# Kernel tuning notes

Hardware: AMD Instinct MI355X
Metric: run time of the kernel (lower is better)

The kernel has to match this reference:

```python
import jax, jax.numpy as jnp
import numpy as np

B, SEQ, PRED, T = 16, 768, 256, 1024
ENC_IN, MARK, D, H, DH = 7, 4, 512, 8, 64
BUCKET, NH, NB = 32, 4, 32          # NB = T // BUCKET (must be even)
DFF, NLAYERS, COUT = 2048, 2, 7
DEC_LEN = 512
MASK_SELF = -5e4                    # reformer TOKEN_SELF_ATTN_VALUE


def setup_inputs():
    key = jax.random.key(0)
    ks = jax.random.split(key, 16)
    s = 0.02
    return {
        "x_enc": jax.random.normal(ks[0], (B, SEQ, ENC_IN), jnp.float32),
        "x_mark_enc": jax.random.normal(ks[1], (B, SEQ, MARK), jnp.float32),
        "x_dec": jax.random.normal(ks[2], (B, DEC_LEN, ENC_IN), jnp.float32),
        "x_mark_dec": jax.random.normal(ks[3], (B, DEC_LEN, MARK), jnp.float32),
        "conv_w": jax.random.normal(ks[4], (D, ENC_IN, 3), jnp.float32) * s,
        "mark_w": jax.random.normal(ks[5], (MARK, D), jnp.float32) * s,
        "qk_w": jax.random.normal(ks[6], (NLAYERS, D, D), jnp.float32) * s,
        "v_w": jax.random.normal(ks[7], (NLAYERS, D, D), jnp.float32) * s,
        "out_w": jax.random.normal(ks[8], (NLAYERS, D, D), jnp.float32) * s,
        "out_b": jnp.zeros((NLAYERS, D), jnp.float32),
        "ln1_g": jnp.ones((NLAYERS, D), jnp.float32),
        "ln1_b": jnp.zeros((NLAYERS, D), jnp.float32),
        "ln2_g": jnp.ones((NLAYERS, D), jnp.float32),
        "ln2_b": jnp.zeros((NLAYERS, D), jnp.float32),
        "ffn_w1": jax.random.normal(ks[9], (NLAYERS, D, DFF), jnp.float32) * s,
        "ffn_b1": jnp.zeros((NLAYERS, DFF), jnp.float32),
        "ffn_w2": jax.random.normal(ks[10], (NLAYERS, DFF, D), jnp.float32) * s,
        "ffn_b2": jnp.zeros((NLAYERS, D), jnp.float32),
        "lnf_g": jnp.ones((D,), jnp.float32),
        "lnf_b": jnp.zeros((D,), jnp.float32),
        "proj_w": jax.random.normal(ks[11], (D, COUT), jnp.float32) * s,
        "proj_b": jnp.zeros((COUT,), jnp.float32),
        "rotations": jax.random.normal(ks[12], (NLAYERS, DH, NH, NB // 2), jnp.float32),
    }


def _layernorm(x, g, b):
    m = x.mean(-1, keepdims=True)
    v = ((x - m) ** 2).mean(-1, keepdims=True)
    return (x - m) / jnp.sqrt(v + 1e-5) * g + b


def _look_one_back(x):
    # concat each chunk with the previous chunk along the within-chunk axis
    return jnp.concatenate([x, jnp.roll(x, 1, axis=1)], axis=2)


def _lsh_attention(qk, v, rot):
    # shared-QK Reformer LSH attention. qk, v: [bh, t, dh]; rot: [dh, NH, NB//2]
    bh, t, d = qk.shape
    nb = t // BUCKET
    rv = jnp.einsum('btf,fhi->bhti', qk, rot)
    rv = jnp.concatenate([rv, -rv], axis=-1)
    buckets = jnp.argmax(rv, axis=-1) + (jnp.arange(NH) * nb)[None, :, None]
    buckets = buckets.reshape(bh, NH * t)                        # [bh, NH*t]
    ticker = jnp.arange(NH * t) % t
    sticker = jnp.argsort(buckets * t + ticker[None, :], axis=-1)
    undo = jnp.argsort(sticker, axis=-1)
    st = sticker % t                                             # source token ids
    sqk = jnp.take_along_axis(qk, st[..., None], axis=1)         # [bh, NH*t, d]
    sv = jnp.take_along_axis(v, st[..., None], axis=1)
    nc = NH * nb                                                 # number of chunks
    bq = sqk.reshape(bh, nc, BUCKET, d)
    bk = bq / jnp.maximum(jnp.linalg.norm(bq, axis=-1, keepdims=True), 1e-12)
    bv = sv.reshape(bh, nc, BUCKET, d)
    bk, bv = _look_one_back(bk), _look_one_back(bv)
    bq_t = st.reshape(bh, nc, BUCKET)
    bkv_t = _look_one_back(bq_t)
    dots = jnp.einsum('bcie,bcje->bcij', bq, bk) * (d ** -0.5)
    dots = jnp.where(bq_t[..., :, None] == bkv_t[..., None, :], MASK_SELF, dots)
    lse = jax.nn.logsumexp(dots, axis=-1, keepdims=True)
    bo = jnp.einsum('bcij,bcje->bcie', jnp.exp(dots - lse), bv)
    so = bo.reshape(bh, NH * t, d)
    sl = lse.reshape(bh, NH * t)
    o = jnp.take_along_axis(so, undo[..., None], axis=1).reshape(bh, NH, t, d)
    logits = jnp.take_along_axis(sl, undo, axis=1).reshape(bh, NH, t, 1)
    return (o * jax.nn.softmax(logits, axis=1)).sum(axis=1)      # [bh, t, d]


def _lsh_self_attn(x, wqk, wv, wo, bo, rot):
    b, t, _ = x.shape
    qk = (x @ wqk).reshape(b, t, H, DH).transpose(0, 2, 1, 3).reshape(b * H, t, DH)
    v = (x @ wv).reshape(b, t, H, DH).transpose(0, 2, 1, 3).reshape(b * H, t, DH)
    o = _lsh_attention(qk, v, rot)
    o = o.reshape(b, H, t, DH).transpose(0, 2, 1, 3).reshape(b, t, D)
    return o @ wo + bo


def _pos_emb(t, d):
    pos = jnp.arange(t, dtype=jnp.float32)[:, None]
    div = jnp.exp(jnp.arange(0, d, 2, dtype=jnp.float32) * (-np.log(10000.0) / d))
    pe = jnp.zeros((t, d), jnp.float32)
    return pe.at[:, 0::2].set(jnp.sin(pos * div)).at[:, 1::2].set(jnp.cos(pos * div))


def _token_emb(x, w):
    # circular Conv1d(enc_in -> d_model, kernel=3, pad=1, no bias)
    t = x.shape[1]
    xp = jnp.concatenate([x[:, -1:], x, x[:, :1]], axis=1)
    return sum(jnp.einsum('bti,oi->bto', xp[:, k:k + t], w[:, :, k]) for k in range(3))


def _forward(x_enc, x_mark_enc, x_dec, x_mark_dec, conv_w, mark_w, qk_w, v_w,
             out_w, out_b, ln1_g, ln1_b, ln2_g, ln2_b, ffn_w1, ffn_b1,
             ffn_w2, ffn_b2, lnf_g, lnf_b, proj_w, proj_b, rotations):
    x = jnp.concatenate([x_enc, x_dec[:, -PRED:, :]], axis=1)       # [B, T, enc_in]
    xm = jnp.concatenate([x_mark_enc, x_mark_dec[:, -PRED:, :]], axis=1)
    h = _token_emb(x, conv_w) + xm @ mark_w + _pos_emb(T, D)[None]  # [B, T, D]
    for l in range(NLAYERS):
        a = _lsh_self_attn(h, qk_w[l], v_w[l], out_w[l], out_b[l], rotations[l])
        h = _layernorm(h + a, ln1_g[l], ln1_b[l])
        y = jax.nn.gelu(h @ ffn_w1[l] + ffn_b1[l], approximate=False) @ ffn_w2[l] + ffn_b2[l]
        h = _layernorm(h + y, ln2_g[l], ln2_b[l])
    h = _layernorm(h, lnf_g, lnf_b)
    out = h @ proj_w + proj_b
    return out[:, -PRED:, :]


def reference(x_enc, x_mark_enc, x_dec, x_mark_dec, conv_w, mark_w, qk_w, v_w,
              out_w, out_b, ln1_g, ln1_b, ln2_g, ln2_b, ffn_w1, ffn_b1,
              ffn_w2, ffn_b2, lnf_g, lnf_b, proj_w, proj_b, rotations):
    return _forward(x_enc, x_mark_enc, x_dec, x_mark_dec, conv_w, mark_w, qk_w, v_w,
                    out_w, out_b, ln1_g, ln1_b, ln2_g, ln2_b, ffn_w1, ffn_b1,
                    ffn_w2, ffn_b2, lnf_g, lnf_b, proj_w, proj_b, rotations)
```

## Files before the change

kernel.cpp:

```cpp
#include <hip/hip_runtime.h>
#include <math.h>

#define T_ 1024
#define NT_ 4096
#define MASKSELF64 -50000.0
#define MASKSELF32 -50000.0f

__global__ __launch_bounds__(256)
void embed_kernel(const float* __restrict__ x_enc, const float* __restrict__ x_mark_enc,
                  const float* __restrict__ x_dec, const float* __restrict__ x_mark_dec,
                  const float* __restrict__ conv_w, const float* __restrict__ mark_w,
                  double* __restrict__ h) {
  int bt = blockIdx.x;
  int b = bt >> 10, t = bt & 1023;
  __shared__ double xs[3][7];
  __shared__ double xm[4];
  int tid = threadIdx.x;
  if (tid < 21) {
    int k = tid / 7, i = tid % 7;
    int tt = t + k - 1;
    if (tt < 0) tt += 1024;
    if (tt >= 1024) tt -= 1024;
    xs[k][i] = (double)((tt < 768) ? x_enc[((size_t)b*768 + tt)*7 + i]
                                   : x_dec[((size_t)b*512 + (tt - 512))*7 + i]);
  }
  if (tid >= 32 && tid < 36) {
    int m = tid - 32;
    xm[m] = (double)((t < 768) ? x_mark_enc[((size_t)b*768 + t)*4 + m]
                               : x_mark_dec[((size_t)b*512 + (t - 512))*4 + m]);
  }
  __syncthreads();
  for (int o = tid; o < 512; o += 256) {
    double acc = 0.0;
    #pragma unroll
    for (int k = 0; k < 3; ++k)
      #pragma unroll
      for (int i = 0; i < 7; ++i)
        acc += xs[k][i] * (double)conv_w[(o*7 + i)*3 + k];
    #pragma unroll
    for (int m = 0; m < 4; ++m) acc += xm[m] * (double)mark_w[m*512 + o];
    int j2 = o & ~1;
    double dv = exp((double)j2 * (-9.210340371976184 / 512.0));
    double arg = (double)t * dv;
    acc += (o & 1) ? cos(arg) : sin(arg);
    h[((size_t)b*1024 + t)*512 + o] = acc;
  }
}

__global__ __launch_bounds__(256)
void dgemm_kernel(const double* __restrict__ A, const float* __restrict__ Bm,
                  const float* __restrict__ bias, double* __restrict__ C,
                  float* __restrict__ C32, int N, int K, int ldb, int flags) {
  __shared__ double As[16][130];
  __shared__ float  Bs[16][132];
  int tid = threadIdx.x;
  int tx = tid & 15, ty = tid >> 4;
  int arow = blockIdx.x * 128;
  int bcol = blockIdx.y * 128;
  int am = tid >> 1, ak = (tid & 1) * 8;
  int bk = tid >> 4, bn = (tid & 15) * 8;
  const double* aptr = A + (size_t)(arow + am)*K + ak;
  const float*  bptr = Bm + (size_t)bk*ldb + bcol + bn;
  double acc[8][8];
  #pragma unroll
  for (int i=0;i<8;++i)
    #pragma unroll
    for (int j=0;j<8;++j) acc[i][j]=0.0;
  double2 av0 = *(const double2*)(aptr + 0);
  double2 av1 = *(const double2*)(aptr + 2);
  double2 av2 = *(const double2*)(aptr + 4);
  double2 av3 = *(const double2*)(aptr + 6);
  float4 bv0 = *(const float4*)(bptr);
  float4 bv1 = *(const float4*)(bptr + 4);
  for (int k0 = 0; k0 < K; k0 += 16) {
    As[ak+0][am] = av0.x; As[ak+1][am] = av0.y;
    As[ak+2][am] = av1.x; As[ak+3][am] = av1.y;
    As[ak+4][am] = av2.x; As[ak+5][am] = av2.y;
    As[ak+6][am] = av3.x; As[ak+7][am] = av3.y;
    *(float4*)&Bs[bk][bn]   = bv0;
    *(float4*)&Bs[bk][bn+4] = bv1;
    __syncthreads();
    if (k0 + 16 < K) {
      aptr += 16;
      bptr += (size_t)16*ldb;
      av0 = *(const double2*)(aptr + 0);
      av1 = *(const double2*)(aptr + 2);
      av2 = *(const double2*)(aptr + 4);
      av3 = *(const double2*)(aptr + 6);
      bv0 = *(const float4*)(bptr);
      bv1 = *(const float4*)(bptr + 4);
    }
    #pragma unroll
    for (int kk=0;kk<16;++kk) {
      double a[8];
      *(double2*)&a[0] = *(const double2*)&As[kk][2*ty];
      *(double2*)&a[2] = *(const double2*)&As[kk][2*ty+32];
      *(double2*)&a[4] = *(const double2*)&As[kk][2*ty+64];
      *(double2*)&a[6] = *(const double2*)&As[kk][2*ty+96];
      float2 f0 = *(const float2*)&Bs[kk][2*tx];
      float2 f1 = *(const float2*)&Bs[kk][2*tx+32];
      float2 f2 = *(const float2*)&Bs[kk][2*tx+64];
      float2 f3 = *(const float2*)&Bs[kk][2*tx+96];
      double b[8];
      b[0]=(double)f0.x; b[1]=(double)f0.y; b[2]=(double)f1.x; b[3]=(double)f1.y;
      b[4]=(double)f2.x; b[5]=(double)f2.y; b[6]=(double)f3.x; b[7]=(double)f3.y;
      #pragma unroll
      for (int i=0;i<8;++i)
        #pragma unroll
        for (int j=0;j<8;++j) acc[i][j] += a[i]*b[j];
    }
    __syncthreads();
  }
  #pragma unroll
  for (int i=0;i<8;++i) {
    int row = arow + 2*ty + (i&1) + 32*(i>>1);
    #pragma unroll
    for (int j=0;j<8;++j) {
      int col = bcol + 2*tx + (j&1) + 32*(j>>1);
      double cv = acc[i][j];
      if (flags & 1) cv += (double)bias[col];
      if (flags & 2) cv = 0.5*cv*(1.0 + erf(cv*0.70710678118654752440));
      if (flags & 4) {
        int b_ = row >> 10, t = row & 1023;
        int hd = col >> 6, dd = col & 63;
        size_t idx = (((size_t)b_*8 + hd)*1024 + t)*64 + dd;
        C[idx] = cv;
        if (flags & 8) C32[idx] = (float)cv;
      } else {
        size_t idx = (size_t)row*N + col;
        if (flags & 16) cv += C[idx];
        C[idx] = cv;
      }
    }
  }
}

__global__ __launch_bounds__(256)
void sgemm_kernel(const float* __restrict__ A, const float* __restrict__ Bm,
                  const float* __restrict__ bias, float* __restrict__ C,
                  int N, int K, int flags) {
  __shared__ float As[16][128];
  __shared__ float Bs[16][128];
  int tid = threadIdx.x;
  int tx = tid & 15, ty = tid >> 4;
  float acc[8][8];
  #pragma unroll
  for (int i=0;i<8;++i)
    #pragma unroll
    for (int j=0;j<8;++j) acc[i][j]=0.f;
  const int arow = blockIdx.x*128;
  const int bcol = blockIdx.y*128;
  int e0 = tid*2, e1 = tid*2 + 1;
  int ra0 = e0 >> 2, ca0 = (e0 & 3)*4;
  int ra1 = e1 >> 2, ca1 = (e1 & 3)*4;
  int kb0 = e0 >> 5, cb0 = (e0 & 31)*4;
  int kb1 = e1 >> 5, cb1 = (e1 & 31)*4;
  const float* pA0 = A + (size_t)(arow + ra0)*K + ca0;
  const float* pA1 = A + (size_t)(arow + ra1)*K + ca1;
  const float* pB0 = Bm + (size_t)kb0*N + bcol + cb0;
  const float* pB1 = Bm + (size_t)kb1*N + bcol + cb1;
  float4 va0 = *(const float4*)pA0;
  float4 va1 = *(const float4*)pA1;
  float4 vb0 = *(const float4*)pB0;
  float4 vb1 = *(const float4*)pB1;
  for (int k0 = 0; k0 < K; k0 += 16) {
    As[ca0+0][ra0]=va0.x; As[ca0+1][ra0]=va0.y; As[ca0+2][ra0]=va0.z; As[ca0+3][ra0]=va0.w;
    As[ca1+0][ra1]=va1.x; As[ca1+1][ra1]=va1.y; As[ca1+2][ra1]=va1.z; As[ca1+3][ra1]=va1.w;
    *(float4*)&Bs[kb0][cb0] = vb0;
    *(float4*)&Bs[kb1][cb1] = vb1;
    __syncthreads();
    if (k0 + 16 < K) {
      pA0 += 16; pA1 += 16;
      pB0 += (size_t)16*N; pB1 += (size_t)16*N;
      va0 = *(const float4*)pA0;
      va1 = *(const float4*)pA1;
      vb0 = *(const float4*)pB0;
      vb1 = *(const float4*)pB1;
    }
    #pragma unroll
    for (int kk=0;kk<16;++kk) {
      float a[8], bb[8];
      #pragma unroll
      for (int i=0;i<8;++i) a[i] = As[kk][ty + 16*i];
      #pragma unroll
      for (int j=0;j<8;++j) bb[j] = Bs[kk][tx + 16*j];
      #pragma unroll
      for (int i=0;i<8;++i)
        #pragma unroll
        for (int j=0;j<8;++j) acc[i][j] += a[i]*bb[j];
    }
    __syncthreads();
  }
  #pragma unroll
  for (int i=0;i<8;++i) {
    int row = arow + ty + 16*i;
    #pragma unroll
    for (int j=0;j<8;++j) {
      int col = bcol + tx + 16*j;
      float cv = acc[i][j];
      if (flags & 1) cv += bias[col];
      if (flags & 2) cv = 0.5f*cv*(1.0f + erff(cv*0.70710678118654752f));
      if (flags & 4) {
        int b = row >> 10, t = row & 1023;
        int hd = col >> 6, dd = col & 63;
        C[(((size_t)b*8 + hd)*1024 + t)*64 + dd] = cv;
      } else {
        C[(size_t)row*N + col] = cv;
      }
    }
  }
}

__global__ __launch_bounds__(256)
void bucket_sort_kernel(const double* __restrict__ qk, const float* __restrict__ rot,
                        int* __restrict__ sticker) {
  int bh = blockIdx.x >> 2, r = blockIdx.x & 3;
  __shared__ double rots[64][17];
  __shared__ unsigned char bucket[1024];
  __shared__ int cnt[32];
  __shared__ int off[32];
  int tid = threadIdx.x;
  for (int idx = tid; idx < 1024; idx += 256) {
    int f = idx >> 4, i = idx & 15;
    rots[f][i] = (double)rot[(f*4 + r)*16 + i];
  }
  if (tid < 32) cnt[tid] = 0;
  __syncthreads();
  for (int t = tid; t < 1024; t += 256) {
    const double* q = qk + ((size_t)bh*1024 + t)*64;
    double rv[16];
    #pragma unroll
    for (int i=0;i<16;++i) rv[i]=0.0;
    for (int f=0; f<64; ++f) {
      double qf = q[f];
      #pragma unroll
      for (int i=0;i<16;++i) rv[i] += qf * rots[f][i];
    }
    int best = 0; double bv = rv[0];
    #pragma unroll
    for (int i=1;i<16;++i) if (rv[i] > bv) { bv=rv[i]; best=i; }
    #pragma unroll
    for (int i=0;i<16;++i) { double nv = -rv[i]; if (nv > bv) { bv=nv; best=16+i; } }
    bucket[t] = (unsigned char)best;
    atomicAdd(&cnt[best], 1);
  }
  __syncthreads();
  if (tid == 0) {
    int s = 0;
    for (int k=0;k<32;++k) { off[k]=s; s+=cnt[k]; }
  }
  __syncthreads();
  if (tid < 32) {
    int pos = off[tid];
    int* outp = sticker + (size_t)bh*NT_ + r*1024;
    for (int t=0;t<1024;++t)
      if (bucket[t] == (unsigned char)tid) outp[pos++] = t;
  }
}

__global__ __launch_bounds__(256)
void lsh_attn_kernel(const double* __restrict__ qk, const double* __restrict__ v,
                     const int* __restrict__ sticker,
                     double* __restrict__ obuf, double* __restrict__ lse, int bh0) {
  int bh_l = blockIdx.x >> 7;
  int bh = bh0 + bh_l;
  int c  = blockIdx.x & 127;
  int cprev = (c + 127) & 127;
  __shared__ double kv[64][66];
  __shared__ double pp[32][66];
  __shared__ double rnorm[64];
  __shared__ int tk[64];
  int tid = threadIdx.x;
  if (tid < 64) {
    int chunk = (tid < 32) ? c : cprev;
    tk[tid] = sticker[(size_t)bh*NT_ + chunk*32 + (tid & 31)];
  }
  __syncthreads();
  for (int idx = tid; idx < 2048; idx += 256) {
    int j = idx >> 5, c2 = (idx & 31)*2;
    *(double2*)&kv[j][c2] = *(const double2*)(qk + ((size_t)bh*1024 + tk[j])*64 + c2);
  }
  __syncthreads();
  if (tid < 64) {
    double s = 0.0;
    #pragma unroll
    for (int f=0; f<64; ++f) { double x = kv[tid][f]; s += x*x; }
    rnorm[tid] = 1.0 / fmax(sqrt(s), 1e-12);
  }
  __syncthreads();
  int i = tid >> 3, sub = tid & 7;
  int ti = tk[i];
  double dots[8];
  double dmax = -1.0e300;
  #pragma unroll
  for (int jj=0; jj<8; ++jj) {
    int j = sub*8 + jj;
    double s = 0.0;
    #pragma unroll
    for (int f=0; f<64; ++f) s += kv[i][f] * kv[j][f];
    s *= rnorm[j] * 0.125;
    if (ti == tk[j]) s = MASKSELF64;
    dots[jj] = s;
    dmax = fmax(dmax, s);
  }
  #pragma unroll
  for (int w=1; w<8; w<<=1) dmax = fmax(dmax, __shfl_xor(dmax, w, 64));
  double esum = 0.0;
  #pragma unroll
  for (int jj=0; jj<8; ++jj) {
    double e = exp(dots[jj] - dmax);
    esum += e;
    pp[i][sub*8+jj] = e;
  }
  #pragma unroll
  for (int w=1; w<8; w<<=1) esum += __shfl_xor(esum, w, 64);
  __syncthreads();
  for (int idx = tid; idx < 2048; idx += 256) {
    int j = idx >> 5, c2 = (idx & 31)*2;
    *(double2*)&kv[j][c2] = *(const double2*)(v + ((size_t)bh*1024 + tk[j])*64 + c2);
  }
  __syncthreads();
  double ov[8];
  #pragma unroll
  for (int dd=0;dd<8;++dd) ov[dd]=0.0;
  for (int j=0;j<64;++j) {
    double p = pp[i][j];
    #pragma unroll
    for (int dd=0;dd<8;++dd) ov[dd] += p * kv[j][sub*8+dd];
  }
  double rinv = 1.0 / esum;
  int r = c >> 5;
  size_t ob = (((size_t)bh_l*4 + r)*1024 + ti)*64 + sub*8;
  #pragma unroll
  for (int dd=0;dd<8;++dd) obuf[ob + dd] = ov[dd]*rinv;
  if (sub == 0) lse[((size_t)bh*4 + r)*1024 + ti] = log(esum) + dmax;
}

__global__ __launch_bounds__(256)
void combine_kernel(const double* __restrict__ obuf, const double* __restrict__ lse,
                    double* __restrict__ comb, int bh0) {
  int g = blockIdx.x*4 + (threadIdx.x >> 6);
  int bh_l = g >> 10, t = g & 1023;
  int bh = bh0 + bh_l;
  int d = threadIdx.x & 63;
  double l[4];
  #pragma unroll
  for (int r=0;r<4;++r) l[r] = lse[((size_t)bh*4 + r)*1024 + t];
  double m = fmax(fmax(l[0],l[1]), fmax(l[2],l[3]));
  double e[4], s=0.0;
  #pragma unroll
  for (int r=0;r<4;++r){ e[r]=exp(l[r]-m); s+=e[r]; }
  double rs = 1.0/s;
  double o = 0.0;
  #pragma unroll
  for (int r=0;r<4;++r)
    o += e[r]*rs * obuf[(((size_t)bh_l*4 + r)*1024 + t)*64 + d];
  int b = bh >> 3, hd = bh & 7;
  comb[((size_t)b*1024 + t)*512 + hd*64 + d] = o;
}

__global__ __launch_bounds__(256)
void lsh_attn32_kernel(const float* __restrict__ qk, const float* __restrict__ v,
                       const int* __restrict__ sticker,
                       float* __restrict__ obuf, float* __restrict__ lse, int bh0) {
  int bh_l = blockIdx.x >> 7;
  int bh = bh0 + bh_l;
  int c  = blockIdx.x & 127;
  int cprev = (c + 127) & 127;
  __shared__ float kv[64][68];
  __shared__ float pp[32][68];
  __shared__ float rnorm[64];
  __shared__ int tk[64];
  int tid = threadIdx.x;
  if (tid < 64) {
    int chunk = (tid < 32) ? c : cprev;
    tk[tid] = sticker[(size_t)bh*NT_ + chunk*32 + (tid & 31)];
  }
  __syncthreads();
  for (int idx = tid; idx < 1024; idx += 256) {
    int j = idx >> 4, c4 = (idx & 15)*4;
    *(float4*)&kv[j][c4] = *(const float4*)(qk + ((size_t)bh*1024 + tk[j])*64 + c4);
  }
  __syncthreads();
  if (tid < 64) {
    float s = 0.f;
    #pragma unroll
    for (int f=0; f<64; ++f) { float x = kv[tid][f]; s += x*x; }
    rnorm[tid] = 1.0f / fmaxf(sqrtf(s), 1e-12f);
  }
  __syncthreads();
  int i = tid >> 3, sub = tid & 7;
  int ti = tk[i];
  float dots[8];
  float dmax = -1.0e30f;
  #pragma unroll
  for (int jj=0; jj<8; ++jj) {
    int j = sub*8 + jj;
    float s = 0.f;
    #pragma unroll
    for (int f=0; f<64; ++f) s += kv[i][f] * kv[j][f];
    s *= rnorm[j] * 0.125f;
    if (ti == tk[j]) s = MASKSELF32;
    dots[jj] = s;
    dmax = fmaxf(dmax, s);
  }
  #pragma unroll
  for (int w=1; w<8; w<<=1) dmax = fmaxf(dmax, __shfl_xor(dmax, w, 64));
  float esum = 0.f;
  #pragma unroll
  for (int jj=0; jj<8; ++jj) {
    float e = expf(dots[jj] - dmax);
    esum += e;
    pp[i][sub*8+jj] = e;
  }
  #pragma unroll
  for (int w=1; w<8; w<<=1) esum += __shfl_xor(esum, w, 64);
  __syncthreads();
  for (int idx = tid; idx < 1024; idx += 256) {
    int j = idx >> 4, c4 = (idx & 15)*4;
    *(float4*)&kv[j][c4] = *(const float4*)(v + ((size_t)bh*1024 + tk[j])*64 + c4);
  }
  __syncthreads();
  float ov[8];
  #pragma unroll
  for (int dd=0;dd<8;++dd) ov[dd]=0.f;
  for (int j=0;j<64;++j) {
    float p = pp[i][j];
    #pragma unroll
    for (int dd=0;dd<8;++dd) ov[dd] += p * kv[j][sub*8+dd];
  }
  float rinv = 1.0f / esum;
  int r = c >> 5;
  size_t ob = (((size_t)bh_l*4 + r)*1024 + ti)*64 + sub*8;
  #pragma unroll
  for (int dd=0;dd<8;++dd) obuf[ob + dd] = ov[dd]*rinv;
  if (sub == 0) lse[((size_t)bh*4 + r)*1024 + ti] = logf(esum) + dmax;
}

__global__ __launch_bounds__(256)
void combine32_kernel(const float* __restrict__ obuf, const float* __restrict__ lse,
                      float* __restrict__ comb, int bh0) {
  int g = blockIdx.x*4 + (threadIdx.x >> 6);
  int bh_l = g >> 10, t = g & 1023;
  int bh = bh0 + bh_l;
  int d = threadIdx.x & 63;
  float l[4];
  #pragma unroll
  for (int r=0;r<4;++r) l[r] = lse[((size_t)bh*4 + r)*1024 + t];
  float m = fmaxf(fmaxf(l[0],l[1]), fmaxf(l[2],l[3]));
  float e[4], s=0.f;
  #pragma unroll
  for (int r=0;r<4;++r){ e[r]=expf(l[r]-m); s+=e[r]; }
  float rs = 1.0f/s;
  float o = 0.f;
  #pragma unroll
  for (int r=0;r<4;++r)
    o += e[r]*rs * obuf[(((size_t)bh_l*4 + r)*1024 + t)*64 + d];
  int b = bh >> 3, hd = bh & 7;
  comb[((size_t)b*1024 + t)*512 + hd*64 + d] = o;
}

__global__ __launch_bounds__(256)
void ln_kernel(const double* __restrict__ x, const double* __restrict__ res,
               const float* __restrict__ gw, const float* __restrict__ bw,
               double* __restrict__ outp, float* __restrict__ out32) {
  int row = blockIdx.x;
  int tid = threadIdx.x;
  const double* xr = x + (size_t)row*512;
  double v0 = xr[tid], v1 = xr[tid+256];
  if (res) { const double* rr = res + (size_t)row*512; v0 += rr[tid]; v1 += rr[tid+256]; }
  double s = v0 + v1;
  #pragma unroll
  for (int w=1; w<64; w<<=1) s += __shfl_xor(s, w, 64);
  __shared__ double red[4];
  int wid = tid >> 6, lane = tid & 63;
  if (lane == 0) red[wid] = s;
  __syncthreads();
  s = red[0]+red[1]+red[2]+red[3];
  double m = s * (1.0/512.0);
  double d0 = v0 - m, d1 = v1 - m;
  double q = d0*d0 + d1*d1;
  #pragma unroll
  for (int w=1; w<64; w<<=1) q += __shfl_xor(q, w, 64);
  __syncthreads();
  if (lane == 0) red[wid] = q;
  __syncthreads();
  q = red[0]+red[1]+red[2]+red[3];
  double var = q * (1.0/512.0);
  double rstd = 1.0 / sqrt(var + 1e-5);
  double o0 = d0*rstd*(double)gw[tid] + (double)bw[tid];
  double o1 = d1*rstd*(double)gw[tid+256] + (double)bw[tid+256];
  outp[(size_t)row*512 + tid]       = o0;
  outp[(size_t)row*512 + tid + 256] = o1;
  if (out32) {
    out32[(size_t)row*512 + tid]       = (float)o0;
    out32[(size_t)row*512 + tid + 256] = (float)o1;
  }
}

__global__ __launch_bounds__(256)
void lnmx_kernel(const double* __restrict__ x, const float* __restrict__ res,
                 const float* __restrict__ gw, const float* __restrict__ bw,
                 float* __restrict__ out32) {
  int row = blockIdx.x;
  int tid = threadIdx.x;
  const double* xr = x + (size_t)row*512;
  const float*  rr = res + (size_t)row*512;
  double v0 = xr[tid] + (double)rr[tid];
  double v1 = xr[tid+256] + (double)rr[tid+256];
  double s = v0 + v1;
  #pragma unroll
  for (int w=1; w<64; w<<=1) s += __shfl_xor(s, w, 64);
  __shared__ double red[4];
  int wid = tid >> 6, lane = tid & 63;
  if (lane == 0) red[wid] = s;
  __syncthreads();
  s = red[0]+red[1]+red[2]+red[3];
  double m = s * (1.0/512.0);
  double d0 = v0 - m, d1 = v1 - m;
  double q = d0*d0 + d1*d1;
  #pragma unroll
  for (int w=1; w<64; w<<=1) q += __shfl_xor(q, w, 64);
  __syncthreads();
  if (lane == 0) red[wid] = q;
  __syncthreads();
  q = red[0]+red[1]+red[2]+red[3];
  double rstd = 1.0 / sqrt(q * (1.0/512.0) + 1e-5);
  out32[(size_t)row*512 + tid]       = (float)(d0*rstd*(double)gw[tid] + (double)bw[tid]);
  out32[(size_t)row*512 + tid + 256] = (float)(d1*rstd*(double)gw[tid+256] + (double)bw[tid+256]);
}

__global__ __launch_bounds__(256)
void ln32_kernel(const float* __restrict__ x, const float* __restrict__ res,
                 const float* __restrict__ gw, const float* __restrict__ bw,
                 float* __restrict__ out32) {
  int row = blockIdx.x;
  int tid = threadIdx.x;
  const float* xr = x + (size_t)row*512;
  double v0 = (double)xr[tid], v1 = (double)xr[tid+256];
  if (res) { const float* rr = res + (size_t)row*512; v0 += (double)rr[tid]; v1 += (double)rr[tid+256]; }
  double s = v0 + v1;
  #pragma unroll
  for (int w=1; w<64; w<<=1) s += __shfl_xor(s, w, 64);
  __shared__ double red[4];
  int wid = tid >> 6, lane = tid & 63;
  if (lane == 0) red[wid] = s;
  __syncthreads();
  s = red[0]+red[1]+red[2]+red[3];
  double m = s * (1.0/512.0);
  double d0 = v0 - m, d1 = v1 - m;
  double q = d0*d0 + d1*d1;
  #pragma unroll
  for (int w=1; w<64; w<<=1) q += __shfl_xor(q, w, 64);
  __syncthreads();
  if (lane == 0) red[wid] = q;
  __syncthreads();
  q = red[0]+red[1]+red[2]+red[3];
  double rstd = 1.0 / sqrt(q * (1.0/512.0) + 1e-5);
  out32[(size_t)row*512 + tid]       = (float)(d0*rstd*(double)gw[tid] + (double)bw[tid]);
  out32[(size_t)row*512 + tid + 256] = (float)(d1*rstd*(double)gw[tid+256] + (double)bw[tid+256]);
}

__global__ __launch_bounds__(64)
void proj_kernel(const float* __restrict__ hf, const float* __restrict__ pw,
                 const float* __restrict__ pb, float* __restrict__ outp) {
  int row = blockIdx.x;
  int b = row >> 8, tp = row & 255;
  const float* hr = hf + ((size_t)b*1024 + 768 + tp)*512;
  int lane = threadIdx.x;
  double acc[7];
  #pragma unroll
  for (int cc=0;cc<7;++cc) acc[cc]=0.0;
  for (int d = lane; d < 512; d += 64) {
    double hv = (double)hr[d];
    #pragma unroll
    for (int cc=0;cc<7;++cc) acc[cc] += hv * (double)pw[d*7 + cc];
  }
  #pragma unroll
  for (int cc=0;cc<7;++cc) {
    double s = acc[cc];
    #pragma unroll
    for (int w=32;w>=1;w>>=1) s += __shfl_xor(s, w, 64);
    if (lane == 0) outp[(size_t)row*7 + cc] = (float)(s + (double)pb[cc]);
  }
}

extern "C" void kernel_launch(void* const* d_in, const int* in_sizes, int n_in,
                              void* d_out, int out_size, void* d_ws, size_t ws_size,
                              hipStream_t stream) {
  (void)in_sizes; (void)n_in; (void)out_size; (void)ws_size;
  const float* x_enc      = (const float*)d_in[0];
  const float* x_mark_enc = (const float*)d_in[1];
  const float* x_dec      = (const float*)d_in[2];
  const float* x_mark_dec = (const float*)d_in[3];
  const float* conv_w     = (const float*)d_in[4];
  const float* mark_w     = (const float*)d_in[5];
  const float* qk_w       = (const float*)d_in[6];
  const float* v_w        = (const float*)d_in[7];
  const float* out_w      = (const float*)d_in[8];
  const float* out_b      = (const float*)d_in[9];
  const float* ln1_g      = (const float*)d_in[10];
  const float* ln1_b      = (const float*)d_in[11];
  const float* ln2_g      = (const float*)d_in[12];
  const float* ln2_b      = (const float*)d_in[13];
  const float* ffn_w1     = (const float*)d_in[14];
  const float* ffn_b1     = (const float*)d_in[15];
  const float* ffn_w2     = (const float*)d_in[16];
  const float* ffn_b2     = (const float*)d_in[17];
  const float* lnf_g      = (const float*)d_in[18];
  const float* lnf_b      = (const float*)d_in[19];
  const float* proj_w     = (const float*)d_in[20];
  const float* proj_b     = (const float*)d_in[21];
  const float* rotations  = (const float*)d_in[22];

  char* ws = (char*)d_ws;
  double* h64   = (double*)(ws);
  double* qk64  = (double*)(ws + 67108864);
  double* v64   = (double*)(ws + 134217728);
  double* obuf  = (double*)(ws + 201326592);
  int*    stick = (int*)   (ws + 234881024);
  double* lse64 = (double*)(ws + 236978176);
  float*  lse32 = (float*) (ws + 236978176);
  double* comb  = v64;
  float* h32    = (float*)(ws + 201326592);
  float* qk32   = (float*)(ws + 134217728);
  float* v32    = (float*)(ws + 167772160);
  float* obuf32 = (float*)(ws + 67108864);
  float* comb32 = (float*)(ws + 100663296);
  float* ao32   = (float*)(ws + 201326592);
  float* hA32   = (float*)(ws + 134217728);
  float* hid32  = (float*)(ws);
  float* y32    = (float*)(ws + 167772160);
  float* h2f    = (float*)(ws + 201326592);
  float* hf32   = (float*)(ws);

  embed_kernel<<<16384, 256, 0, stream>>>(x_enc, x_mark_enc, x_dec, x_mark_dec,
                                          conv_w, mark_w, h64);

  dgemm_kernel<<<dim3(128,4), 256, 0, stream>>>(h64, qk_w, nullptr, qk64, nullptr,
                                                512, 512, 512, 4);
  dgemm_kernel<<<dim3(128,4), 256, 0, stream>>>(h64, v_w, nullptr, v64, nullptr,
                                                512, 512, 512, 4);
  bucket_sort_kernel<<<512, 256, 0, stream>>>(qk64, rotations, stick);
  for (int g = 0; g < 8; ++g) {
    lsh_attn_kernel<<<2048, 256, 0, stream>>>(qk64, v64, stick, obuf, lse64, g*16);
    combine_kernel<<<4096, 256, 0, stream>>>(obuf, lse64, comb, g*16);
  }
  dgemm_kernel<<<dim3(128,4), 256, 0, stream>>>(comb, out_w, out_b, qk64, nullptr,
                                                512, 512, 512, 1);
  ln_kernel<<<16384, 256, 0, stream>>>(h64, qk64, ln1_g, ln1_b, h64, nullptr);
  for (int c = 0; c < 4; ++c) {
    dgemm_kernel<<<dim3(128,4), 256, 0, stream>>>(h64, ffn_w1 + c*512,
                                                  ffn_b1 + c*512, qk64, nullptr,
                                                  512, 512, 2048, 3);
    dgemm_kernel<<<dim3(128,4), 256, 0, stream>>>(qk64, ffn_w2 + (size_t)c*512*512,
                                                  ffn_b2, comb, nullptr,
                                                  512, 512, 512, (c == 0) ? 1 : 16);
  }
  ln_kernel<<<16384, 256, 0, stream>>>(h64, comb, ln2_g, ln2_b, h64, h32);

  sgemm_kernel<<<dim3(128,4), 256, 0, stream>>>(h32, v_w + 262144, nullptr, v32,
                                                512, 512, 4);
  dgemm_kernel<<<dim3(128,4), 256, 0, stream>>>(h64, qk_w + 262144, nullptr, qk64, qk32,
                                                512, 512, 512, 4 | 8);
  bucket_sort_kernel<<<512, 256, 0, stream>>>(qk64, rotations + 4096, stick);
  for (int g = 0; g < 4; ++g) {
    lsh_attn32_kernel<<<4096, 256, 0, stream>>>(qk32, v32, stick, obuf32, lse32, g*32);
    combine32_kernel<<<8192, 256, 0, stream>>>(obuf32, lse32, comb32, g*32);
  }
  sgemm_kernel<<<dim3(128,4), 256, 0, stream>>>(comb32, out_w + 262144, out_b + 512,
                                                ao32, 512, 512, 1);
  lnmx_kernel<<<16384, 256, 0, stream>>>(h64, ao32, ln1_g + 512, ln1_b + 512, hA32);
  sgemm_kernel<<<dim3(128,16), 256, 0, stream>>>(hA32, ffn_w1 + 1048576, ffn_b1 + 2048,
                                                 hid32, 2048, 512, 3);
  sgemm_kernel<<<dim3(128,4), 256, 0, stream>>>(hid32, ffn_w2 + 1048576, ffn_b2 + 512,
                                                y32, 512, 2048, 1);
  ln32_kernel<<<16384, 256, 0, stream>>>(hA32, y32, ln2_g + 512, ln2_b + 512, h2f);
  ln32_kernel<<<16384, 256, 0, stream>>>(h2f, nullptr, lnf_g, lnf_b, hf32);
  proj_kernel<<<4096, 64, 0, stream>>>(hf32, proj_w, proj_b, (float*)d_out);
}
```

Baseline: 5.487 ms.

## Use bf16 MFMA GEMMs for layer-2 FFN and parallelize bucket scatter

Replaces the two fp32 SIMT GEMMs of the second-layer FFN with a bf16 MFMA kernel (16x16x32), converting weights to transposed bf16 each call and emitting bf16 activations from the preceding layernorm and GELU epilogue. Separately, the bucket sort's serial 32-thread scatter over all 1024 tokens is replaced by per-chunk histograms and prefix offsets, so 512 threads each scan only 64 tokens. The bf16 path trades accuracy for matrix-core throughput, and the weight conversion adds work to every call.

```diff
diff --git a/kernel.cpp b/kernel.cpp
--- a/kernel.cpp
+++ b/kernel.cpp
@@ -5,6 +5,14 @@
 #define NT_ 4096
 #define MASKSELF64 -50000.0
 #define MASKSELF32 -50000.0f
+
+typedef short bf16x8 __attribute__((ext_vector_type(8)));
+typedef float f32x4 __attribute__((ext_vector_type(4)));
+
+__device__ __forceinline__ unsigned short f2bf(float f) {
+  unsigned int x = __float_as_uint(f);
+  return (unsigned short)((x + 0x7FFFu + ((x >> 16) & 1u)) >> 16);
+}
 
 __global__ __launch_bounds__(256)
 void embed_kernel(const float* __restrict__ x_enc, const float* __restrict__ x_mark_enc,
@@ -212,19 +220,99 @@
 }
 
 __global__ __launch_bounds__(256)
+void convert_wt_kernel(const float* __restrict__ w, unsigned short* __restrict__ wt,
+                       int K, int N) {
+  int total = K * N;
+  for (int i = blockIdx.x*256 + threadIdx.x; i < total; i += gridDim.x*256) {
+    int n = i / K, k = i - n*K;
+    wt[i] = f2bf(w[(size_t)k*N + n]);
+  }
+}
+
+__global__ __launch_bounds__(256)
+void bgemm_kernel(const unsigned short* __restrict__ A, const unsigned short* __restrict__ Bt,
+                  const float* __restrict__ bias, float* __restrict__ Cf,
+                  unsigned short* __restrict__ C16, int N, int K, int flags) {
+  __shared__ unsigned short As[128*32];
+  __shared__ unsigned short Bs[128*32];
+  int tid = threadIdx.x;
+  int lane = tid & 63, wave = tid >> 6;
+  int wr = wave >> 1, wc = wave & 1;
+  int l15 = lane & 15, l4 = lane >> 4;
+  int arow = blockIdx.x * 128, bcol = blockIdx.y * 128;
+  int s0 = tid, s1 = tid + 256;
+  int r0 = s0 >> 2, q0 = s0 & 3;
+  int r1 = s1 >> 2, q1 = s1 & 3;
+  const unsigned short* pA0 = A + (size_t)(arow + r0)*K + q0*8;
+  const unsigned short* pA1 = A + (size_t)(arow + r1)*K + q1*8;
+  const unsigned short* pB0 = Bt + (size_t)(bcol + r0)*K + q0*8;
+  const unsigned short* pB1 = Bt + (size_t)(bcol + r1)*K + q1*8;
+  f32x4 acc[4][4];
+  #pragma unroll
+  for (int i=0;i<4;++i)
+    #pragma unroll
+    for (int j=0;j<4;++j)
+      #pragma unroll
+      for (int r=0;r<4;++r) acc[i][j][r] = 0.f;
+  uint4 a0 = *(const uint4*)pA0, a1 = *(const uint4*)pA1;
+  uint4 b0 = *(const uint4*)pB0, b1 = *(const uint4*)pB1;
+  for (int k0 = 0; k0 < K; k0 += 32) {
+    *(uint4*)&As[r0*32 + q0*8] = a0;
+    *(uint4*)&As[r1*32 + q1*8] = a1;
+    *(uint4*)&Bs[r0*32 + q0*8] = b0;
+    *(uint4*)&Bs[r1*32 + q1*8] = b1;
+    __syncthreads();
+    if (k0 + 32 < K) {
+      pA0 += 32; pA1 += 32; pB0 += 32; pB1 += 32;
+      a0 = *(const uint4*)pA0; a1 = *(const uint4*)pA1;
+      b0 = *(const uint4*)pB0; b1 = *(const uint4*)pB1;
+    }
+    bf16x8 aF[4], bF[4];
+    #pragma unroll
+    for (int mt=0; mt<4; ++mt)
+      aF[mt] = *(const bf16x8*)&As[(wr*64 + mt*16 + l15)*32 + l4*8];
+    #pragma unroll
+    for (int nt=0; nt<4; ++nt)
+      bF[nt] = *(const bf16x8*)&Bs[(wc*64 + nt*16 + l15)*32 + l4*8];
+    #pragma unroll
+    for (int mt=0; mt<4; ++mt)
+      #pragma unroll
+      for (int nt=0; nt<4; ++nt)
+        acc[mt][nt] = __builtin_amdgcn_mfma_f32_16x16x32_bf16(aF[mt], bF[nt], acc[mt][nt], 0, 0, 0);
+    __syncthreads();
+  }
+  #pragma unroll
+  for (int mt=0; mt<4; ++mt) {
+    #pragma unroll
+    for (int nt=0; nt<4; ++nt) {
+      int col = bcol + wc*64 + nt*16 + l15;
+      float bv = (flags & 1) ? bias[col] : 0.f;
+      #pragma unroll
+      for (int r=0; r<4; ++r) {
+        int row = arow + wr*64 + mt*16 + l4*4 + r;
+        float cv = acc[mt][nt][r] + bv;
+        if (flags & 2) cv = 0.5f*cv*(1.0f + erff(cv*0.70710678118654752f));
+        if (flags & 8) C16[(size_t)row*N + col] = f2bf(cv);
+        else           Cf[(size_t)row*N + col] = cv;
+      }
+    }
+  }
+}
+
+__global__ __launch_bounds__(256)
 void bucket_sort_kernel(const double* __restrict__ qk, const float* __restrict__ rot,
                         int* __restrict__ sticker) {
   int bh = blockIdx.x >> 2, r = blockIdx.x & 3;
   __shared__ double rots[64][17];
   __shared__ unsigned char bucket[1024];
   __shared__ int cnt[32];
-  __shared__ int off[32];
+  __shared__ short H[16][32];
+  __shared__ int off2[16][32];
   int tid = threadIdx.x;
   for (int idx = tid; idx < 1024; idx += 256) {
     int f = idx >> 4, i = idx & 15;
     rots[f][i] = (double)rot[(f*4 + r)*16 + i];
   }
-  if (tid < 32) cnt[tid] = 0;
   __syncthreads();
   for (int t = tid; t < 1024; t += 256) {
     const double* q = qk + ((size_t)bh*1024 + t)*64;
@@ -242,19 +330,40 @@
     #pragma unroll
     for (int i=0;i<16;++i) { double nv = -rv[i]; if (nv > bv) { bv=nv; best=16+i; } }
     bucket[t] = (unsigned char)best;
-    atomicAdd(&cnt[best], 1);
-  }
-  __syncthreads();
-  if (tid == 0) {
+  }
+  __syncthreads();
+  {
+    int c = tid >> 4, s = tid & 15;
+    int h0 = 0, h1 = 0;
+    for (int t = c*64; t < c*64 + 64; ++t) {
+      int b = bucket[t];
+      h0 += (b == s);
+      h1 += (b == s + 16);
+    }
+    H[c][s] = (short)h0;
+    H[c][s+16] = (short)h1;
+  }
+  __syncthreads();
+  if (tid < 32) {
     int s = 0;
-    for (int k=0;k<32;++k) { off[k]=s; s+=cnt[k]; }
+    for (int c = 0; c < 16; ++c) s += H[c][tid];
+    cnt[tid] = s;
   }
   __syncthreads();
   if (tid < 32) {
-    int pos = off[tid];
-    int* outp = sticker + (size_t)bh*NT_ + r*1024;
-    for (int t=0;t<1024;++t)
-      if (bucket[t] == (unsigned char)tid) outp[pos++] = t;
+    int o = 0;
+    for (int b = 0; b < tid; ++b) o += cnt[b];
+    for (int c = 0; c < 16; ++c) { off2[c][tid] = o; o += H[c][tid]; }
+  }
+  __syncthreads();
+  int* outp = sticker + (size_t)bh*NT_ + r*1024;
+  #pragma unroll
+  for (int q = 0; q < 2; ++q) {
+    int p = tid + q*256;
+    int c = p >> 5, b = p & 31;
+    int pos = off2[c][b];
+    for (int t = c*64; t < c*64 + 64; ++t)
+      if (bucket[t] == (unsigned char)b) outp[pos++] = t;
   }
 }
 
@@ -501,7 +610,7 @@
 __global__ __launch_bounds__(256)
 void lnmx_kernel(const double* __restrict__ x, const float* __restrict__ res,
                  const float* __restrict__ gw, const float* __restrict__ bw,
-                 float* __restrict__ out32) {
+                 float* __restrict__ out32, unsigned short* __restrict__ out16) {
   int row = blockIdx.x;
   int tid = threadIdx.x;
   const double* xr = x + (size_t)row*512;
@@ -526,8 +635,12 @@
   __syncthreads();
   q = red[0]+red[1]+red[2]+red[3];
   double rstd = 1.0 / sqrt(q * (1.0/512.0) + 1e-5);
-  out32[(size_t)row*512 + tid]       = (float)(d0*rstd*(double)gw[tid] + (double)bw[tid]);
-  out32[(size_t)row*512 + tid + 256] = (float)(d1*rstd*(double)gw[tid+256] + (double)bw[tid+256]);
+  float o0 = (float)(d0*rstd*(double)gw[tid] + (double)bw[tid]);
+  float o1 = (float)(d1*rstd*(double)gw[tid+256] + (double)bw[tid+256]);
+  out32[(size_t)row*512 + tid]       = o0;
+  out32[(size_t)row*512 + tid + 256] = o1;
+  out16[(size_t)row*512 + tid]       = f2bf(o0);
+  out16[(size_t)row*512 + tid + 256] = f2bf(o1);
 }
 
 __global__ __launch_bounds__(256)
@@ -621,6 +734,8 @@
   int*    stick = (int*)   (ws + 234881024);
   double* lse64 = (double*)(ws + 236978176);
   float*  lse32 = (float*) (ws + 236978176);
+  unsigned short* w1t = (unsigned short*)(ws + 241172480);
+  unsigned short* w2t = (unsigned short*)(ws + 243269632);
   double* comb  = v64;
   float* h32    = (float*)(ws + 201326592);
   float* qk32   = (float*)(ws + 134217728);
@@ -629,13 +744,16 @@
   float* comb32 = (float*)(ws + 100663296);
   float* ao32   = (float*)(ws + 201326592);
   float* hA32   = (float*)(ws + 134217728);
-  float* hid32  = (float*)(ws);
+  unsigned short* hA16  = (unsigned short*)(ws + 67108864);
+  unsigned short* hid16 = (unsigned short*)(ws);
   float* y32    = (float*)(ws + 167772160);
   float* h2f    = (float*)(ws + 201326592);
-  float* hf32   = (float*)(ws);
+  float* hf32   = (float*)(ws + 67108864);
 
   embed_kernel<<<16384, 256, 0, stream>>>(x_enc, x_mark_enc, x_dec, x_mark_dec,
                                           conv_w, mark_w, h64);
+  convert_wt_kernel<<<2048, 256, 0, stream>>>(ffn_w1 + 1048576, w1t, 512, 2048);
+  convert_wt_kernel<<<2048, 256, 0, stream>>>(ffn_w2 + 1048576, w2t, 2048, 512);
 
   dgemm_kernel<<<dim3(128,4), 256, 0, stream>>>(h64, qk_w, nullptr, qk64, nullptr,
                                                 512, 512, 512, 4);
@@ -670,11 +788,11 @@
   }
   sgemm_kernel<<<dim3(128,4), 256, 0, stream>>>(comb32, out_w + 262144, out_b + 512,
                                                 ao32, 512, 512, 1);
-  lnmx_kernel<<<16384, 256, 0, stream>>>(h64, ao32, ln1_g + 512, ln1_b + 512, hA32);
-  sgemm_kernel<<<dim3(128,16), 256, 0, stream>>>(hA32, ffn_w1 + 1048576, ffn_b1 + 2048,
-                                                 hid32, 2048, 512, 3);
-  sgemm_kernel<<<dim3(128,4), 256, 0, stream>>>(hid32, ffn_w2 + 1048576, ffn_b2 + 512,
-                                                y32, 512, 2048, 1);
+  lnmx_kernel<<<16384, 256, 0, stream>>>(h64, ao32, ln1_g + 512, ln1_b + 512, hA32, hA16);
+  bgemm_kernel<<<dim3(128,16), 256, 0, stream>>>(hA16, w1t, ffn_b1 + 2048,
+                                                 nullptr, hid16, 2048, 512, 1|2|8);
+  bgemm_kernel<<<dim3(128,4), 256, 0, stream>>>(hid16, w2t, ffn_b2 + 512,
+                                                y32, nullptr, 512, 2048, 1);
   ln32_kernel<<<16384, 256, 0, stream>>>(hA32, y32, ln2_g + 512, ln2_b + 512, h2f);
   ln32_kernel<<<16384, 256, 0, stream>>>(h2f, nullptr, lnf_g, lnf_b, hf32);
   proj_kernel<<<4096, 64, 0, stream>>>(hf32, proj_w, proj_b, (float*)d_out);
```

New measurement: 4.608 ms. 1.19x faster.
